# Kernel optimization log

Measured on AMD Instinct MI355X. Metric: run time of the kernel, lower is better.

Reference implementation:

```python
import jax, jax.numpy as jnp
import numpy as np

NUM_ITEMS = 100000
HIDDEN = 128
NNZ = 1600000


def setup_inputs() -> dict:
    key = jax.random.key(0)
    k1, k2, k3, k4, k5, k6 = jax.random.split(key, 6)
    item_embedding_table = jax.random.normal(k1, (NUM_ITEMS, HIDDEN), dtype=jnp.float32)
    adj_rows = jnp.sort(jax.random.randint(k2, (NNZ,), 0, NUM_ITEMS, dtype=jnp.int32))
    adj_cols = jax.random.randint(k3, (NNZ,), 0, NUM_ITEMS, dtype=jnp.int32)
    adj_vals = jax.random.uniform(k4, (NNZ,), dtype=jnp.float32)
    # nn.Linear default init (uniform in +-1/sqrt(fan_in)) approximated by scaled normal
    W_weight = jax.random.normal(k5, (HIDDEN, HIDDEN), dtype=jnp.float32) / np.sqrt(HIDDEN)
    W_bias = jax.random.normal(k6, (HIDDEN,), dtype=jnp.float32) * 0.01
    return {
        "item_embedding_table": item_embedding_table,
        "adj_rows": adj_rows,
        "adj_cols": adj_cols,
        "adj_vals": adj_vals,
        "W_weight": W_weight,
        "W_bias": W_bias,
    }


def reference(item_embedding_table, adj_rows, adj_cols, adj_vals, W_weight, W_bias):
    # support = W(x): x @ W^T + b   (nn.Linear convention: weight [out, in])
    support = jnp.einsum("nd,hd->nh", item_embedding_table, W_weight) + W_bias  # [N, H]
    # output = sparse_coo(adj) @ support, via gather + segment-sum scatter
    msgs = adj_vals[:, None] * support[adj_cols]  # [nnz, H]
    output = jax.ops.segment_sum(msgs, adj_rows, num_segments=NUM_ITEMS)  # [N, H]
    return output
```

## Files before the change

### kernel.cpp

```cpp
#include <hip/hip_runtime.h>
#include <hip/hip_fp16.h>

#define N_ITEMS 100000
#define HID 128
#define NNZ_T 1600000
#define PREPW_BLOCKS 64
#define RP_BLOCKS 391

typedef unsigned short ushort_t;
typedef unsigned int uint_t;
typedef short bf16x8 __attribute__((ext_vector_type(8)));
typedef float f32x4 __attribute__((ext_vector_type(4)));

static __device__ __forceinline__ ushort_t f32_to_bf16(float f) {
    uint_t u = __float_as_uint(f);
    uint_t r = (u + 0x7FFFu + ((u >> 16) & 1u)) >> 16;
    return (ushort_t)r;
}

__global__ void prep(const float* __restrict__ W, const int* __restrict__ rows,
                     ushort_t* __restrict__ Wb, int* __restrict__ row_ptr) {
    if (blockIdx.x < PREPW_BLOCKS) {
        int i = blockIdx.x * 256 + threadIdx.x;
        Wb[i] = f32_to_bf16(W[i]);
        return;
    }
    int r = (blockIdx.x - PREPW_BLOCKS) * 256 + threadIdx.x;
    if (r > N_ITEMS) return;
    int lo = 0, hi = NNZ_T;
    while (lo < hi) {
        int mid = (lo + hi) >> 1;
        if (rows[mid] < r) lo = mid + 1; else hi = mid;
    }
    row_ptr[r] = lo;
}

__global__ __launch_bounds__(256) void gemm_mfma(
    const float* __restrict__ X, const ushort_t* __restrict__ Wb,
    const float* __restrict__ bias, ushort_t* __restrict__ S) {
    const int lane = threadIdx.x & 63;
    const int wave = threadIdx.x >> 6;
    const int m = lane & 15;
    const int q = lane >> 4;
    const int row0 = blockIdx.x * 64 + wave * 16;

    int arow = row0 + m;
    if (arow >= N_ITEMS) arow = N_ITEMS - 1;

    f32x4 acc[8] = {};

#pragma unroll
    for (int kb = 0; kb < 4; ++kb) {
        const int k0 = kb * 32 + q * 8;
        float4 a0 = *(const float4*)&X[(size_t)arow * HID + k0];
        float4 a1 = *(const float4*)&X[(size_t)arow * HID + k0 + 4];
        bf16x8 xf;
        xf[0] = (short)f32_to_bf16(a0.x); xf[1] = (short)f32_to_bf16(a0.y);
        xf[2] = (short)f32_to_bf16(a0.z); xf[3] = (short)f32_to_bf16(a0.w);
        xf[4] = (short)f32_to_bf16(a1.x); xf[5] = (short)f32_to_bf16(a1.y);
        xf[6] = (short)f32_to_bf16(a1.z); xf[7] = (short)f32_to_bf16(a1.w);
#pragma unroll
        for (int nt = 0; nt < 8; ++nt) {
            bf16x8 wf = *(const bf16x8*)&Wb[(size_t)(nt * 16 + m) * HID + k0];
            acc[nt] = __builtin_amdgcn_mfma_f32_16x16x32_bf16(wf, xf, acc[nt], 0, 0, 0);
        }
    }

    const int srow = row0 + m;
    const bool ok = srow < N_ITEMS;
#pragma unroll
    for (int nt = 0; nt < 8; ++nt) {
        const int c0 = nt * 16 + q * 4;
        float4 bv = *(const float4*)&bias[c0];
        ushort_t h0 = __half_as_ushort(__float2half(acc[nt][0] + bv.x));
        ushort_t h1 = __half_as_ushort(__float2half(acc[nt][1] + bv.y));
        ushort_t h2 = __half_as_ushort(__float2half(acc[nt][2] + bv.z));
        ushort_t h3 = __half_as_ushort(__float2half(acc[nt][3] + bv.w));
        uint2 pk;
        pk.x = (uint_t)h0 | ((uint_t)h1 << 16);
        pk.y = (uint_t)h2 | ((uint_t)h3 << 16);
        if (ok) *(uint2*)&S[(size_t)srow * HID + c0] = pk;
    }
}

__global__ __launch_bounds__(256) void spmm_csr(
    const int* __restrict__ cols, const float* __restrict__ vals,
    const int* __restrict__ row_ptr, const ushort_t* __restrict__ S,
    float* __restrict__ out) {
    const int lane = threadIdx.x & 63;
    const int wid = blockIdx.x * 4 + ((threadIdx.x >> 6) & 3);
    const int r0 = wid * 2;
    if (r0 >= N_ITEMS) return;

    const int g = lane >> 4;
    const int l = lane & 15;
    const int sel = lane >> 5;

    const int2 p01 = *(const int2*)&row_ptr[r0];
    const int pEb = row_ptr[r0 + 2];
    int pa = p01.x; const int pEa = p01.y;
    int pb = p01.y;

    __half2 accA[4], accB[4];
#pragma unroll
    for (int j = 0; j < 4; ++j) { accA[j] = __float2half2_rn(0.f); accB[j] = __float2half2_rn(0.f); }

    while (pa < pEa || pb < pEb) {
        const int base = sel ? pb : pa;
        const int end  = sel ? pEb : pEa;
        const int idx  = base + (lane & 15);
        const int cidx = max(min(idx, end - 1), 0);
        const int c_l  = cols[cidx];
        const float v_l = (idx < end) ? vals[cidx] : 0.f;

        uint4 uA[4], uB[4];
        float vA[4], vB[4];
#pragma unroll
        for (int t = 0; t < 4; ++t) {
            const int sa = 4 * t + g;
            const int ca = __shfl(c_l, sa, 64);
            vA[t] = __shfl(v_l, sa, 64);
            uA[t] = *(const uint4*)&S[(size_t)ca * HID + 8 * l];
            const int cb = __shfl(c_l, 32 + sa, 64);
            vB[t] = __shfl(v_l, 32 + sa, 64);
            uB[t] = *(const uint4*)&S[(size_t)cb * HID + 8 * l];
        }
#pragma unroll
        for (int t = 0; t < 4; ++t) {
            const __half2 wa = __float2half2_rn(vA[t]);
            accA[0] = __hfma2(wa, *(const __half2*)&uA[t].x, accA[0]);
            accA[1] = __hfma2(wa, *(const __half2*)&uA[t].y, accA[1]);
            accA[2] = __hfma2(wa, *(const __half2*)&uA[t].z, accA[2]);
            accA[3] = __hfma2(wa, *(const __half2*)&uA[t].w, accA[3]);
            const __half2 wb = __float2half2_rn(vB[t]);
            accB[0] = __hfma2(wb, *(const __half2*)&uB[t].x, accB[0]);
            accB[1] = __hfma2(wb, *(const __half2*)&uB[t].y, accB[1]);
            accB[2] = __hfma2(wb, *(const __half2*)&uB[t].z, accB[2]);
            accB[3] = __hfma2(wb, *(const __half2*)&uB[t].w, accB[3]);
        }
        pa = min(pa + 16, pEa);
        pb = min(pb + 16, pEb);
    }

    float fA[8], fB[8];
#pragma unroll
    for (int j = 0; j < 4; ++j) {
        fA[2 * j] = __low2float(accA[j]);  fA[2 * j + 1] = __high2float(accA[j]);
        fB[2 * j] = __low2float(accB[j]);  fB[2 * j + 1] = __high2float(accB[j]);
    }
#pragma unroll
    for (int e = 0; e < 8; ++e) {
        fA[e] += __shfl_xor(fA[e], 16, 64);
        fA[e] += __shfl_xor(fA[e], 32, 64);
        fB[e] += __shfl_xor(fB[e], 16, 64);
        fB[e] += __shfl_xor(fB[e], 32, 64);
    }
    if (g == 0) {
        float* p = &out[(size_t)r0 * HID + 8 * l];
        *(float4*)p       = make_float4(fA[0], fA[1], fA[2], fA[3]);
        *(float4*)(p + 4) = make_float4(fA[4], fA[5], fA[6], fA[7]);
    } else if (g == 1 && r0 + 1 < N_ITEMS) {
        float* p = &out[(size_t)(r0 + 1) * HID + 8 * l];
        *(float4*)p       = make_float4(fB[0], fB[1], fB[2], fB[3]);
        *(float4*)(p + 4) = make_float4(fB[4], fB[5], fB[6], fB[7]);
    }
}

extern "C" void kernel_launch(void* const* d_in, const int* in_sizes, int n_in,
                              void* d_out, int out_size, void* d_ws, size_t ws_size,
                              hipStream_t stream) {
    const float* X    = (const float*)d_in[0];
    const int*   rows = (const int*)  d_in[1];
    const int*   cols = (const int*)  d_in[2];
    const float* vals = (const float*)d_in[3];
    const float* W    = (const float*)d_in[4];
    const float* bias = (const float*)d_in[5];
    float* out = (float*)d_out;

    ushort_t* Wb      = (ushort_t*)d_ws;
    ushort_t* S       = Wb + HID * HID;
    int*      row_ptr = (int*)(S + (size_t)N_ITEMS * HID);

    prep<<<PREPW_BLOCKS + RP_BLOCKS, 256, 0, stream>>>(W, rows, Wb, row_ptr);
    gemm_mfma<<<(N_ITEMS + 63) / 64, 256, 0, stream>>>(X, Wb, bias, S);
    spmm_csr<<<(N_ITEMS / 2 + 3) / 4, 256, 0, stream>>>(cols, vals, row_ptr, S, out);
}
```

Before: 203.1 us.

## Fuse prep into GEMM with LDS-staged W; persistent prefetching SpMM

Merges the W-conversion/row_ptr kernel with the GEMM so there is one fewer launch. Each GEMM block converts W to bf16 into swizzled shared memory instead of reading a global bf16 copy. The SpMM becomes a persistent grid-stride kernel that prefetches the next row pair's row_ptr and the next chunk's cols/vals while processing the current chunk, hiding index-load latency. The cost is redundant W conversion in every GEMM block, 32KB of LDS per block, and a fixed 2048-block SpMM grid that may balance load less evenly.

Measured after the change: 188.5 us. 1.08x faster.

```diff
diff --git a/kernel.cpp b/kernel.cpp
--- a/kernel.cpp
+++ b/kernel.cpp
@@ -4,8 +4,10 @@
 #define N_ITEMS 100000
 #define HID 128
 #define NNZ_T 1600000
-#define PREPW_BLOCKS 64
 #define RP_BLOCKS 391
+#define GB_BLOCKS 1563
+#define SPMM_BLOCKS 2048
+#define WSTRIDE (SPMM_BLOCKS * 4)
 
 typedef unsigned short ushort_t;
 typedef unsigned int uint_t;
@@ -18,35 +20,52 @@
     return (ushort_t)r;
 }
 
-__global__ void prep(const float* __restrict__ W, const int* __restrict__ rows,
-                     ushort_t* __restrict__ Wb, int* __restrict__ row_ptr) {
-    if (blockIdx.x < PREPW_BLOCKS) {
-        int i = blockIdx.x * 256 + threadIdx.x;
-        Wb[i] = f32_to_bf16(W[i]);
+__global__ __launch_bounds__(256) void prep_gemm(
+    const float* __restrict__ X, const float* __restrict__ W,
+    const float* __restrict__ bias, const int* __restrict__ rows,
+    ushort_t* __restrict__ S, int* __restrict__ row_ptr) {
+    if (blockIdx.x < RP_BLOCKS) {
+        int r = blockIdx.x * 256 + threadIdx.x;
+        if (r > N_ITEMS) return;
+        int lo = 0, hi = NNZ_T;
+        while (lo < hi) {
+            int mid = (lo + hi) >> 1;
+            if (rows[mid] < r) lo = mid + 1; else hi = mid;
+        }
+        row_ptr[r] = lo;
         return;
     }
-    int r = (blockIdx.x - PREPW_BLOCKS) * 256 + threadIdx.x;
-    if (r > N_ITEMS) return;
-    int lo = 0, hi = NNZ_T;
-    while (lo < hi) {
-        int mid = (lo + hi) >> 1;
-        if (rows[mid] < r) lo = mid + 1; else hi = mid;
-    }
-    row_ptr[r] = lo;
-}
-
-__global__ __launch_bounds__(256) void gemm_mfma(
-    const float* __restrict__ X, const ushort_t* __restrict__ Wb,
-    const float* __restrict__ bias, ushort_t* __restrict__ S) {
+
+    __shared__ ushort_t Wl[HID * HID];
+    {
+        const int t = threadIdx.x;
+        const float4* Wf = (const float4*)W;
+#pragma unroll
+        for (int j = 0; j < 8; ++j) {
+            const int gblk = j * 256 + t;
+            float4 w0 = Wf[gblk * 2];
+            float4 w1 = Wf[gblk * 2 + 1];
+            bf16x8 v;
+            v[0] = (short)f32_to_bf16(w0.x); v[1] = (short)f32_to_bf16(w0.y);
+            v[2] = (short)f32_to_bf16(w0.z); v[3] = (short)f32_to_bf16(w0.w);
+            v[4] = (short)f32_to_bf16(w1.x); v[5] = (short)f32_to_bf16(w1.y);
+            v[6] = (short)f32_to_bf16(w1.z); v[7] = (short)f32_to_bf16(w1.w);
+            const int ps = (gblk * 8) ^ (((gblk >> 4) & 7) << 3);
+            *(bf16x8*)&Wl[ps] = v;
+        }
+    }
+    __syncthreads();
+
     const int lane = threadIdx.x & 63;
     const int wave = threadIdx.x >> 6;
     const int m = lane & 15;
     const int q = lane >> 4;
-    const int row0 = blockIdx.x * 64 + wave * 16;
+    const int row0 = (blockIdx.x - RP_BLOCKS) * 64 + wave * 16;
 
     int arow = row0 + m;
     if (arow >= N_ITEMS) arow = N_ITEMS - 1;
 
+    const int swz = (m & 7) << 3;
     f32x4 acc[8] = {};
 
 #pragma unroll
@@ -61,7 +80,7 @@
         xf[6] = (short)f32_to_bf16(a1.z); xf[7] = (short)f32_to_bf16(a1.w);
 #pragma unroll
         for (int nt = 0; nt < 8; ++nt) {
-            bf16x8 wf = *(const bf16x8*)&Wb[(size_t)(nt * 16 + m) * HID + k0];
+            const bf16x8 wf = *(const bf16x8*)&Wl[((nt * 16 + m) * HID + k0) ^ swz];
             acc[nt] = __builtin_amdgcn_mfma_f32_16x16x32_bf16(wf, xf, acc[nt], 0, 0, 0);
         }
     }
@@ -88,81 +107,110 @@
     const int* __restrict__ row_ptr, const ushort_t* __restrict__ S,
     float* __restrict__ out) {
     const int lane = threadIdx.x & 63;
-    const int wid = blockIdx.x * 4 + ((threadIdx.x >> 6) & 3);
-    const int r0 = wid * 2;
-    if (r0 >= N_ITEMS) return;
-
     const int g = lane >> 4;
     const int l = lane & 15;
     const int sel = lane >> 5;
-
-    const int2 p01 = *(const int2*)&row_ptr[r0];
-    const int pEb = row_ptr[r0 + 2];
-    int pa = p01.x; const int pEa = p01.y;
-    int pb = p01.y;
-
-    __half2 accA[4], accB[4];
-#pragma unroll
-    for (int j = 0; j < 4; ++j) { accA[j] = __float2half2_rn(0.f); accB[j] = __float2half2_rn(0.f); }
-
-    while (pa < pEa || pb < pEb) {
-        const int base = sel ? pb : pa;
-        const int end  = sel ? pEb : pEa;
-        const int idx  = base + (lane & 15);
-        const int cidx = max(min(idx, end - 1), 0);
-        const int c_l  = cols[cidx];
-        const float v_l = (idx < end) ? vals[cidx] : 0.f;
-
-        uint4 uA[4], uB[4];
-        float vA[4], vB[4];
-#pragma unroll
-        for (int t = 0; t < 4; ++t) {
-            const int sa = 4 * t + g;
-            const int ca = __shfl(c_l, sa, 64);
-            vA[t] = __shfl(v_l, sa, 64);
-            uA[t] = *(const uint4*)&S[(size_t)ca * HID + 8 * l];
-            const int cb = __shfl(c_l, 32 + sa, 64);
-            vB[t] = __shfl(v_l, 32 + sa, 64);
-            uB[t] = *(const uint4*)&S[(size_t)cb * HID + 8 * l];
-        }
-#pragma unroll
-        for (int t = 0; t < 4; ++t) {
-            const __half2 wa = __float2half2_rn(vA[t]);
-            accA[0] = __hfma2(wa, *(const __half2*)&uA[t].x, accA[0]);
-            accA[1] = __hfma2(wa, *(const __half2*)&uA[t].y, accA[1]);
-            accA[2] = __hfma2(wa, *(const __half2*)&uA[t].z, accA[2]);
-            accA[3] = __hfma2(wa, *(const __half2*)&uA[t].w, accA[3]);
-            const __half2 wb = __float2half2_rn(vB[t]);
-            accB[0] = __hfma2(wb, *(const __half2*)&uB[t].x, accB[0]);
-            accB[1] = __hfma2(wb, *(const __half2*)&uB[t].y, accB[1]);
-            accB[2] = __hfma2(wb, *(const __half2*)&uB[t].z, accB[2]);
-            accB[3] = __hfma2(wb, *(const __half2*)&uB[t].w, accB[3]);
-        }
-        pa = min(pa + 16, pEa);
-        pb = min(pb + 16, pEb);
-    }
-
-    float fA[8], fB[8];
-#pragma unroll
-    for (int j = 0; j < 4; ++j) {
-        fA[2 * j] = __low2float(accA[j]);  fA[2 * j + 1] = __high2float(accA[j]);
-        fB[2 * j] = __low2float(accB[j]);  fB[2 * j + 1] = __high2float(accB[j]);
-    }
-#pragma unroll
-    for (int e = 0; e < 8; ++e) {
-        fA[e] += __shfl_xor(fA[e], 16, 64);
-        fA[e] += __shfl_xor(fA[e], 32, 64);
-        fB[e] += __shfl_xor(fB[e], 16, 64);
-        fB[e] += __shfl_xor(fB[e], 32, 64);
-    }
-    if (g == 0) {
-        float* p = &out[(size_t)r0 * HID + 8 * l];
-        *(float4*)p       = make_float4(fA[0], fA[1], fA[2], fA[3]);
-        *(float4*)(p + 4) = make_float4(fA[4], fA[5], fA[6], fA[7]);
-    } else if (g == 1 && r0 + 1 < N_ITEMS) {
-        float* p = &out[(size_t)(r0 + 1) * HID + 8 * l];
-        *(float4*)p       = make_float4(fB[0], fB[1], fB[2], fB[3]);
-        *(float4*)(p + 4) = make_float4(fB[4], fB[5], fB[6], fB[7]);
+    const int NP = N_ITEMS / 2;
+
+    int wid = blockIdx.x * 4 + (threadIdx.x >> 6);
+    if (wid >= NP) return;
+    int2 p01 = *(const int2*)&row_ptr[wid * 2];
+    int pE2 = row_ptr[wid * 2 + 2];
+
+    for (;;) {
+        const int nwid = wid + WSTRIDE;
+        const bool has_next = (nwid < NP);
+        int2 np01 = p01; int npE2 = pE2;
+        if (has_next) {
+            np01 = *(const int2*)&row_ptr[nwid * 2];
+            npE2 = row_ptr[nwid * 2 + 2];
+        }
+
+        int pa = p01.x; const int pEa = p01.y;
+        int pb = p01.y; const int pEb = pE2;
+
+        __half2 accA[4], accB[4];
+#pragma unroll
+        for (int j = 0; j < 4; ++j) { accA[j] = __float2half2_rn(0.f); accB[j] = __float2half2_rn(0.f); }
+
+        if (pa < pEa || pb < pEb) {
+            const int base = sel ? pb : pa;
+            const int end  = sel ? pEb : pEa;
+            const int idx  = base + l;
+            const int cidx = max(min(idx, end - 1), 0);
+            int   c_l = cols[cidx];
+            float v_l = (idx < end) ? vals[cidx] : 0.f;
+
+            for (;;) {
+                const int pa2 = min(pa + 16, pEa);
+                const int pb2 = min(pb + 16, pEb);
+                const bool more = (pa2 < pEa) || (pb2 < pEb);
+                int c_n = 0; float v_n = 0.f;
+                if (more) {
+                    const int b2 = sel ? pb2 : pa2;
+                    const int e2 = sel ? pEb : pEa;
+                    const int i2 = b2 + l;
+                    const int ci2 = max(min(i2, e2 - 1), 0);
+                    c_n = cols[ci2];
+                    v_n = (i2 < e2) ? vals[ci2] : 0.f;
+                }
+
+                uint4 uA[4], uB[4];
+                float vA[4], vB[4];
+#pragma unroll
+                for (int t = 0; t < 4; ++t) {
+                    const int sa = 4 * t + g;
+                    const int ca = __shfl(c_l, sa, 64);
+                    vA[t] = __shfl(v_l, sa, 64);
+                    uA[t] = *(const uint4*)&S[(size_t)ca * HID + 8 * l];
+                    const int cb = __shfl(c_l, 32 + sa, 64);
+                    vB[t] = __shfl(v_l, 32 + sa, 64);
+                    uB[t] = *(const uint4*)&S[(size_t)cb * HID + 8 * l];
+                }
+#pragma unroll
+                for (int t = 0; t < 4; ++t) {
+                    const __half2 wa = __float2half2_rn(vA[t]);
+                    accA[0] = __hfma2(wa, *(const __half2*)&uA[t].x, accA[0]);
+                    accA[1] = __hfma2(wa, *(const __half2*)&uA[t].y, accA[1]);
+                    accA[2] = __hfma2(wa, *(const __half2*)&uA[t].z, accA[2]);
+                    accA[3] = __hfma2(wa, *(const __half2*)&uA[t].w, accA[3]);
+                    const __half2 wb = __float2half2_rn(vB[t]);
+                    accB[0] = __hfma2(wb, *(const __half2*)&uB[t].x, accB[0]);
+                    accB[1] = __hfma2(wb, *(const __half2*)&uB[t].y, accB[1]);
+                    accB[2] = __hfma2(wb, *(const __half2*)&uB[t].z, accB[2]);
+                    accB[3] = __hfma2(wb, *(const __half2*)&uB[t].w, accB[3]);
+                }
+                if (!more) break;
+                pa = pa2; pb = pb2; c_l = c_n; v_l = v_n;
+            }
+        }
+
+        float fA[8], fB[8];
+#pragma unroll
+        for (int j = 0; j < 4; ++j) {
+            fA[2 * j] = __low2float(accA[j]);  fA[2 * j + 1] = __high2float(accA[j]);
+            fB[2 * j] = __low2float(accB[j]);  fB[2 * j + 1] = __high2float(accB[j]);
+        }
+#pragma unroll
+        for (int e = 0; e < 8; ++e) {
+            fA[e] += __shfl_xor(fA[e], 16, 64);
+            fA[e] += __shfl_xor(fA[e], 32, 64);
+            fB[e] += __shfl_xor(fB[e], 16, 64);
+            fB[e] += __shfl_xor(fB[e], 32, 64);
+        }
+        const int r0 = wid * 2;
+        if (g == 0) {
+            float* p = &out[(size_t)r0 * HID + 8 * l];
+            *(float4*)p       = make_float4(fA[0], fA[1], fA[2], fA[3]);
+            *(float4*)(p + 4) = make_float4(fA[4], fA[5], fA[6], fA[7]);
+        } else if (g == 1 && r0 + 1 < N_ITEMS) {
+            float* p = &out[(size_t)(r0 + 1) * HID + 8 * l];
+            *(float4*)p       = make_float4(fB[0], fB[1], fB[2], fB[3]);
+            *(float4*)(p + 4) = make_float4(fB[4], fB[5], fB[6], fB[7]);
+        }
+
+        if (!has_next) break;
+        wid = nwid; p01 = np01; pE2 = npE2;
     }
 }
 
@@ -177,11 +225,9 @@
     const float* bias = (const float*)d_in[5];
     float* out = (float*)d_out;
 
-    ushort_t* Wb      = (ushort_t*)d_ws;
-    ushort_t* S       = Wb + HID * HID;
+    ushort_t* S       = (ushort_t*)d_ws;
     int*      row_ptr = (int*)(S + (size_t)N_ITEMS * HID);
 
-    prep<<<PREPW_BLOCKS + RP_BLOCKS, 256, 0, stream>>>(W, rows, Wb, row_ptr);
-    gemm_mfma<<<(N_ITEMS + 63) / 64, 256, 0, stream>>>(X, Wb, bias, S);
-    spmm_csr<<<(N_ITEMS / 2 + 3) / 4, 256, 0, stream>>>(cols, vals, row_ptr, S, out);
-}
+    prep_gemm<<<RP_BLOCKS + GB_BLOCKS, 256, 0, stream>>>(X, W, bias, rows, S, row_ptr);
+    spmm_csr<<<SPMM_BLOCKS, 256, 0, stream>>>(cols, vals, row_ptr, S, out);
+}
```

## Fuse prep, GEMM and SpMM into one persistent cooperative kernel with grid sync

Applied to the files above, without the earlier changes.

Merges the three kernels into a single persistent cooperative kernel. Each block builds row_ptr with a grid-stride loop, converts W to bf16 into swizzled LDS, and runs grid-strided GEMM tiles. After a grid-wide sync it runs grid-strided SpMM rows. This removes two kernel launch boundaries and the global Wb round trip, at the cost of a grid barrier, lower occupancy from the 32KB LDS and launch bounds, and every block redundantly converting W.

New measurement: 319.7 us. +57.4%, slower.

```diff
diff --git a/kernel.cpp b/kernel.cpp
--- a/kernel.cpp
+++ b/kernel.cpp
@@ -1,11 +1,14 @@
 #include <hip/hip_runtime.h>
 #include <hip/hip_fp16.h>
+#include <hip/hip_cooperative_groups.h>
+
+namespace cg = cooperative_groups;
 
 #define N_ITEMS 100000
 #define HID 128
 #define NNZ_T 1600000
-#define PREPW_BLOCKS 64
-#define RP_BLOCKS 391
+#define GEMM_TILES 1563
+#define MAX_BLOCKS 1024
 
 typedef unsigned short ushort_t;
 typedef unsigned int uint_t;
@@ -18,151 +21,165 @@
     return (ushort_t)r;
 }
 
-__global__ void prep(const float* __restrict__ W, const int* __restrict__ rows,
-                     ushort_t* __restrict__ Wb, int* __restrict__ row_ptr) {
-    if (blockIdx.x < PREPW_BLOCKS) {
-        int i = blockIdx.x * 256 + threadIdx.x;
-        Wb[i] = f32_to_bf16(W[i]);
-        return;
-    }
-    int r = (blockIdx.x - PREPW_BLOCKS) * 256 + threadIdx.x;
-    if (r > N_ITEMS) return;
-    int lo = 0, hi = NNZ_T;
-    while (lo < hi) {
-        int mid = (lo + hi) >> 1;
-        if (rows[mid] < r) lo = mid + 1; else hi = mid;
-    }
-    row_ptr[r] = lo;
-}
-
-__global__ __launch_bounds__(256) void gemm_mfma(
-    const float* __restrict__ X, const ushort_t* __restrict__ Wb,
-    const float* __restrict__ bias, ushort_t* __restrict__ S) {
-    const int lane = threadIdx.x & 63;
-    const int wave = threadIdx.x >> 6;
+__global__ __launch_bounds__(256, 4) void gcn_fused(
+    const float* __restrict__ X, const int* __restrict__ rows,
+    const int* __restrict__ cols, const float* __restrict__ vals,
+    const float* __restrict__ W, const float* __restrict__ bias,
+    ushort_t* __restrict__ S, int* __restrict__ row_ptr,
+    float* __restrict__ out, int nblocks) {
+
+    const int tid = threadIdx.x;
+    const int lane = tid & 63;
+    const int wave = tid >> 6;
+
+    for (int r = blockIdx.x * 256 + tid; r <= N_ITEMS; r += nblocks * 256) {
+        int lo = 0, hi = NNZ_T;
+        while (lo < hi) {
+            int mid = (lo + hi) >> 1;
+            if (rows[mid] < r) lo = mid + 1; else hi = mid;
+        }
+        row_ptr[r] = lo;
+    }
+
+    __shared__ ushort_t Wl[HID * HID];
+    {
+        const float4* Wf = (const float4*)W;
+#pragma unroll
+        for (int j = 0; j < 8; ++j) {
+            const int gblk = j * 256 + tid;
+            float4 w0 = Wf[gblk * 2];
+            float4 w1 = Wf[gblk * 2 + 1];
+            bf16x8 v;
+            v[0] = (short)f32_to_bf16(w0.x); v[1] = (short)f32_to_bf16(w0.y);
+            v[2] = (short)f32_to_bf16(w0.z); v[3] = (short)f32_to_bf16(w0.w);
+            v[4] = (short)f32_to_bf16(w1.x); v[5] = (short)f32_to_bf16(w1.y);
+            v[6] = (short)f32_to_bf16(w1.z); v[7] = (short)f32_to_bf16(w1.w);
+            const int ps = (gblk * 8) ^ (((gblk >> 4) & 7) << 3);
+            *(bf16x8*)&Wl[ps] = v;
+        }
+    }
+    __syncthreads();
+
     const int m = lane & 15;
     const int q = lane >> 4;
-    const int row0 = blockIdx.x * 64 + wave * 16;
-
-    int arow = row0 + m;
-    if (arow >= N_ITEMS) arow = N_ITEMS - 1;
-
-    f32x4 acc[8] = {};
-
-#pragma unroll
-    for (int kb = 0; kb < 4; ++kb) {
-        const int k0 = kb * 32 + q * 8;
-        float4 a0 = *(const float4*)&X[(size_t)arow * HID + k0];
-        float4 a1 = *(const float4*)&X[(size_t)arow * HID + k0 + 4];
-        bf16x8 xf;
-        xf[0] = (short)f32_to_bf16(a0.x); xf[1] = (short)f32_to_bf16(a0.y);
-        xf[2] = (short)f32_to_bf16(a0.z); xf[3] = (short)f32_to_bf16(a0.w);
-        xf[4] = (short)f32_to_bf16(a1.x); xf[5] = (short)f32_to_bf16(a1.y);
-        xf[6] = (short)f32_to_bf16(a1.z); xf[7] = (short)f32_to_bf16(a1.w);
+    const int swz = (m & 7) << 3;
+    for (int tile = blockIdx.x; tile < GEMM_TILES; tile += nblocks) {
+        const int row0 = tile * 64 + wave * 16;
+        int arow = row0 + m;
+        if (arow >= N_ITEMS) arow = N_ITEMS - 1;
+
+        f32x4 acc[8] = {};
+#pragma unroll
+        for (int kb = 0; kb < 4; ++kb) {
+            const int k0 = kb * 32 + q * 8;
+            float4 a0 = *(const float4*)&X[(size_t)arow * HID + k0];
+            float4 a1 = *(const float4*)&X[(size_t)arow * HID + k0 + 4];
+            bf16x8 xf;
+            xf[0] = (short)f32_to_bf16(a0.x); xf[1] = (short)f32_to_bf16(a0.y);
+            xf[2] = (short)f32_to_bf16(a0.z); xf[3] = (short)f32_to_bf16(a0.w);
+            xf[4] = (short)f32_to_bf16(a1.x); xf[5] = (short)f32_to_bf16(a1.y);
+            xf[6] = (short)f32_to_bf16(a1.z); xf[7] = (short)f32_to_bf16(a1.w);
+#pragma unroll
+            for (int nt = 0; nt < 8; ++nt) {
+                const bf16x8 wf = *(const bf16x8*)&Wl[((nt * 16 + m) * HID + k0) ^ swz];
+                acc[nt] = __builtin_amdgcn_mfma_f32_16x16x32_bf16(wf, xf, acc[nt], 0, 0, 0);
+            }
+        }
+
+        const int srow = row0 + m;
+        const bool ok = srow < N_ITEMS;
 #pragma unroll
         for (int nt = 0; nt < 8; ++nt) {
-            bf16x8 wf = *(const bf16x8*)&Wb[(size_t)(nt * 16 + m) * HID + k0];
-            acc[nt] = __builtin_amdgcn_mfma_f32_16x16x32_bf16(wf, xf, acc[nt], 0, 0, 0);
-        }
-    }
-
-    const int srow = row0 + m;
-    const bool ok = srow < N_ITEMS;
-#pragma unroll
-    for (int nt = 0; nt < 8; ++nt) {
-        const int c0 = nt * 16 + q * 4;
-        float4 bv = *(const float4*)&bias[c0];
-        ushort_t h0 = __half_as_ushort(__float2half(acc[nt][0] + bv.x));
-        ushort_t h1 = __half_as_ushort(__float2half(acc[nt][1] + bv.y));
-        ushort_t h2 = __half_as_ushort(__float2half(acc[nt][2] + bv.z));
-        ushort_t h3 = __half_as_ushort(__float2half(acc[nt][3] + bv.w));
-        uint2 pk;
-        pk.x = (uint_t)h0 | ((uint_t)h1 << 16);
-        pk.y = (uint_t)h2 | ((uint_t)h3 << 16);
-        if (ok) *(uint2*)&S[(size_t)srow * HID + c0] = pk;
-    }
-}
-
-__global__ __launch_bounds__(256) void spmm_csr(
-    const int* __restrict__ cols, const float* __restrict__ vals,
-    const int* __restrict__ row_ptr, const ushort_t* __restrict__ S,
-    float* __restrict__ out) {
-    const int lane = threadIdx.x & 63;
-    const int wid = blockIdx.x * 4 + ((threadIdx.x >> 6) & 3);
-    const int r0 = wid * 2;
-    if (r0 >= N_ITEMS) return;
+            const int c0 = nt * 16 + q * 4;
+            float4 bv = *(const float4*)&bias[c0];
+            ushort_t h0 = __half_as_ushort(__float2half(acc[nt][0] + bv.x));
+            ushort_t h1 = __half_as_ushort(__float2half(acc[nt][1] + bv.y));
+            ushort_t h2 = __half_as_ushort(__float2half(acc[nt][2] + bv.z));
+            ushort_t h3 = __half_as_ushort(__float2half(acc[nt][3] + bv.w));
+            uint2 pk;
+            pk.x = (uint_t)h0 | ((uint_t)h1 << 16);
+            pk.y = (uint_t)h2 | ((uint_t)h3 << 16);
+            if (ok) *(uint2*)&S[(size_t)srow * HID + c0] = pk;
+        }
+    }
+
+    cg::this_grid().sync();
 
     const int g = lane >> 4;
     const int l = lane & 15;
     const int sel = lane >> 5;
-
-    const int2 p01 = *(const int2*)&row_ptr[r0];
-    const int pEb = row_ptr[r0 + 2];
-    int pa = p01.x; const int pEa = p01.y;
-    int pb = p01.y;
-
-    __half2 accA[4], accB[4];
-#pragma unroll
-    for (int j = 0; j < 4; ++j) { accA[j] = __float2half2_rn(0.f); accB[j] = __float2half2_rn(0.f); }
-
-    while (pa < pEa || pb < pEb) {
-        const int base = sel ? pb : pa;
-        const int end  = sel ? pEb : pEa;
-        const int idx  = base + (lane & 15);
-        const int cidx = max(min(idx, end - 1), 0);
-        const int c_l  = cols[cidx];
-        const float v_l = (idx < end) ? vals[cidx] : 0.f;
-
-        uint4 uA[4], uB[4];
-        float vA[4], vB[4];
-#pragma unroll
-        for (int t = 0; t < 4; ++t) {
-            const int sa = 4 * t + g;
-            const int ca = __shfl(c_l, sa, 64);
-            vA[t] = __shfl(v_l, sa, 64);
-            uA[t] = *(const uint4*)&S[(size_t)ca * HID + 8 * l];
-            const int cb = __shfl(c_l, 32 + sa, 64);
-            vB[t] = __shfl(v_l, 32 + sa, 64);
-            uB[t] = *(const uint4*)&S[(size_t)cb * HID + 8 * l];
-        }
-#pragma unroll
-        for (int t = 0; t < 4; ++t) {
-            const __half2 wa = __float2half2_rn(vA[t]);
-            accA[0] = __hfma2(wa, *(const __half2*)&uA[t].x, accA[0]);
-            accA[1] = __hfma2(wa, *(const __half2*)&uA[t].y, accA[1]);
-            accA[2] = __hfma2(wa, *(const __half2*)&uA[t].z, accA[2]);
-            accA[3] = __hfma2(wa, *(const __half2*)&uA[t].w, accA[3]);
-            const __half2 wb = __float2half2_rn(vB[t]);
-            accB[0] = __hfma2(wb, *(const __half2*)&uB[t].x, accB[0]);
-            accB[1] = __hfma2(wb, *(const __half2*)&uB[t].y, accB[1]);
-            accB[2] = __hfma2(wb, *(const __half2*)&uB[t].z, accB[2]);
-            accB[3] = __hfma2(wb, *(const __half2*)&uB[t].w, accB[3]);
-        }
-        pa = min(pa + 16, pEa);
-        pb = min(pb + 16, pEb);
-    }
-
-    float fA[8], fB[8];
-#pragma unroll
-    for (int j = 0; j < 4; ++j) {
-        fA[2 * j] = __low2float(accA[j]);  fA[2 * j + 1] = __high2float(accA[j]);
-        fB[2 * j] = __low2float(accB[j]);  fB[2 * j + 1] = __high2float(accB[j]);
-    }
-#pragma unroll
-    for (int e = 0; e < 8; ++e) {
-        fA[e] += __shfl_xor(fA[e], 16, 64);
-        fA[e] += __shfl_xor(fA[e], 32, 64);
-        fB[e] += __shfl_xor(fB[e], 16, 64);
-        fB[e] += __shfl_xor(fB[e], 32, 64);
-    }
-    if (g == 0) {
-        float* p = &out[(size_t)r0 * HID + 8 * l];
-        *(float4*)p       = make_float4(fA[0], fA[1], fA[2], fA[3]);
-        *(float4*)(p + 4) = make_float4(fA[4], fA[5], fA[6], fA[7]);
-    } else if (g == 1 && r0 + 1 < N_ITEMS) {
-        float* p = &out[(size_t)(r0 + 1) * HID + 8 * l];
-        *(float4*)p       = make_float4(fB[0], fB[1], fB[2], fB[3]);
-        *(float4*)(p + 4) = make_float4(fB[4], fB[5], fB[6], fB[7]);
+    const int nwaves = nblocks * 4;
+
+    for (int wid = blockIdx.x * 4 + wave; wid < N_ITEMS / 2; wid += nwaves) {
+        const int r0 = wid * 2;
+        const int2 p01 = *(const int2*)&row_ptr[r0];
+        const int pEb = row_ptr[r0 + 2];
+        int pa = p01.x; const int pEa = p01.y;
+        int pb = p01.y;
+
+        __half2 accA[4], accB[4];
+#pragma unroll
+        for (int j = 0; j < 4; ++j) { accA[j] = __float2half2_rn(0.f); accB[j] = __float2half2_rn(0.f); }
+
+        while (pa < pEa || pb < pEb) {
+            const int base = sel ? pb : pa;
+            const int end  = sel ? pEb : pEa;
+            const int idx  = base + (lane & 15);
+            const int cidx = max(min(idx, end - 1), 0);
+            const int c_l  = cols[cidx];
+            const float v_l = (idx < end) ? vals[cidx] : 0.f;
+
+            uint4 uA[4], uB[4];
+            float vA[4], vB[4];
+#pragma unroll
+            for (int t = 0; t < 4; ++t) {
+                const int sa = 4 * t + g;
+                const int ca = __shfl(c_l, sa, 64);
+                vA[t] = __shfl(v_l, sa, 64);
+                uA[t] = *(const uint4*)&S[(size_t)ca * HID + 8 * l];
+                const int cb = __shfl(c_l, 32 + sa, 64);
+                vB[t] = __shfl(v_l, 32 + sa, 64);
+                uB[t] = *(const uint4*)&S[(size_t)cb * HID + 8 * l];
+            }
+#pragma unroll
+            for (int t = 0; t < 4; ++t) {
+                const __half2 wa = __float2half2_rn(vA[t]);
+                accA[0] = __hfma2(wa, *(const __half2*)&uA[t].x, accA[0]);
+                accA[1] = __hfma2(wa, *(const __half2*)&uA[t].y, accA[1]);
+                accA[2] = __hfma2(wa, *(const __half2*)&uA[t].z, accA[2]);
+                accA[3] = __hfma2(wa, *(const __half2*)&uA[t].w, accA[3]);
+                const __half2 wb = __float2half2_rn(vB[t]);
+                accB[0] = __hfma2(wb, *(const __half2*)&uB[t].x, accB[0]);
+                accB[1] = __hfma2(wb, *(const __half2*)&uB[t].y, accB[1]);
+                accB[2] = __hfma2(wb, *(const __half2*)&uB[t].z, accB[2]);
+                accB[3] = __hfma2(wb, *(const __half2*)&uB[t].w, accB[3]);
+            }
+            pa = min(pa + 16, pEa);
+            pb = min(pb + 16, pEb);
+        }
+
+        float fA[8], fB[8];
+#pragma unroll
+        for (int j = 0; j < 4; ++j) {
+            fA[2 * j] = __low2float(accA[j]);  fA[2 * j + 1] = __high2float(accA[j]);
+            fB[2 * j] = __low2float(accB[j]);  fB[2 * j + 1] = __high2float(accB[j]);
+        }
+#pragma unroll
+        for (int e = 0; e < 8; ++e) {
+            fA[e] += __shfl_xor(fA[e], 16, 64);
+            fA[e] += __shfl_xor(fA[e], 32, 64);
+            fB[e] += __shfl_xor(fB[e], 16, 64);
+            fB[e] += __shfl_xor(fB[e], 32, 64);
+        }
+        if (g == 0) {
+            float* p = &out[(size_t)r0 * HID + 8 * l];
+            *(float4*)p       = make_float4(fA[0], fA[1], fA[2], fA[3]);
+            *(float4*)(p + 4) = make_float4(fA[4], fA[5], fA[6], fA[7]);
+        } else if (g == 1 && r0 + 1 < N_ITEMS) {
+            float* p = &out[(size_t)(r0 + 1) * HID + 8 * l];
+            *(float4*)p       = make_float4(fB[0], fB[1], fB[2], fB[3]);
+            *(float4*)(p + 4) = make_float4(fB[4], fB[5], fB[6], fB[7]);
+        }
     }
 }
 
@@ -177,11 +194,26 @@
     const float* bias = (const float*)d_in[5];
     float* out = (float*)d_out;
 
-    ushort_t* Wb      = (ushort_t*)d_ws;
-    ushort_t* S       = Wb + HID * HID;
+    ushort_t* S       = (ushort_t*)d_ws;
     int*      row_ptr = (int*)(S + (size_t)N_ITEMS * HID);
 
-    prep<<<PREPW_BLOCKS + RP_BLOCKS, 256, 0, stream>>>(W, rows, Wb, row_ptr);
-    gemm_mfma<<<(N_ITEMS + 63) / 64, 256, 0, stream>>>(X, Wb, bias, S);
-    spmm_csr<<<(N_ITEMS / 2 + 3) / 4, 256, 0, stream>>>(cols, vals, row_ptr, S, out);
+    static int nblocks = 0;
+    if (nblocks == 0) {
+        int per_cu = 0;
+        hipOccupancyMaxActiveBlocksPerMultiprocessor(
+            &per_cu, reinterpret_cast<const void*>(gcn_fused), 256, 0);
+        int num_cu = 256;
+        hipDeviceProp_t prop;
+        if (hipGetDeviceProperties(&prop, 0) == hipSuccess && prop.multiProcessorCount > 0)
+            num_cu = prop.multiProcessorCount;
+        nblocks = (per_cu > 0 ? per_cu : 1) * num_cu;
+        if (nblocks > MAX_BLOCKS) nblocks = MAX_BLOCKS;
+        if (nblocks < 256) nblocks = 256;
+    }
+
+    void* args[] = {(void*)&X, (void*)&rows, (void*)&cols, (void*)&vals,
+                    (void*)&W, (void*)&bias, (void*)&S, (void*)&row_ptr,
+                    (void*)&out, (void*)&nblocks};
+    hipLaunchCooperativeKernel(reinterpret_cast<void*>(gcn_fused),
+                               dim3(nblocks), dim3(256), args, 0, stream);
 }
```

## Fuse row-pointer prep and GEMM into one persistent kernel with LDS weights

Applied to the files above, without the earlier changes.

Merges the prep and GEMM launches into one kernel. Some blocks compute CSR row pointers while the rest convert W to bf16 into swizzled shared memory and loop persistently over GEMM tiles. This removes one kernel launch and the global bf16 weight buffer. Nontemporal loads and stores are also added for X, the gathered S rows and the output. The risk is that nontemporal hints on the gathered S rows lower cache reuse, and each GEMM block pays a 32KB LDS fill.

New measurement: 208.1 us. 2.5% more time.

```diff
diff --git a/kernel.cpp b/kernel.cpp
--- a/kernel.cpp
+++ b/kernel.cpp
@@ -4,13 +4,17 @@
 #define N_ITEMS 100000
 #define HID 128
 #define NNZ_T 1600000
-#define PREPW_BLOCKS 64
 #define RP_BLOCKS 391
+#define GEMM_TILES 1563
+#define GEMM_BLOCKS 781
+#define SPMM_BLOCKS 12500
 
 typedef unsigned short ushort_t;
 typedef unsigned int uint_t;
 typedef short bf16x8 __attribute__((ext_vector_type(8)));
 typedef float f32x4 __attribute__((ext_vector_type(4)));
+typedef float f32x4v __attribute__((ext_vector_type(4)));
+typedef uint_t u32x4v __attribute__((ext_vector_type(4)));
 
 static __device__ __forceinline__ ushort_t f32_to_bf16(float f) {
     uint_t u = __float_as_uint(f);
@@ -18,68 +22,90 @@
     return (ushort_t)r;
 }
 
-__global__ void prep(const float* __restrict__ W, const int* __restrict__ rows,
-                     ushort_t* __restrict__ Wb, int* __restrict__ row_ptr) {
-    if (blockIdx.x < PREPW_BLOCKS) {
-        int i = blockIdx.x * 256 + threadIdx.x;
-        Wb[i] = f32_to_bf16(W[i]);
+static __device__ __forceinline__ __half2 u2h2(uint_t w) {
+    union { uint_t u; __half2 h; } c; c.u = w; return c.h;
+}
+
+__global__ __launch_bounds__(256) void prep_gemm(
+    const float* __restrict__ X, const float* __restrict__ W,
+    const float* __restrict__ bias, const int* __restrict__ rows,
+    ushort_t* __restrict__ S, int* __restrict__ row_ptr) {
+    if (blockIdx.x < RP_BLOCKS) {
+        int r = blockIdx.x * 256 + threadIdx.x;
+        if (r > N_ITEMS) return;
+        int lo = 0, hi = NNZ_T;
+        while (lo < hi) {
+            int mid = (lo + hi) >> 1;
+            if (rows[mid] < r) lo = mid + 1; else hi = mid;
+        }
+        row_ptr[r] = lo;
         return;
     }
-    int r = (blockIdx.x - PREPW_BLOCKS) * 256 + threadIdx.x;
-    if (r > N_ITEMS) return;
-    int lo = 0, hi = NNZ_T;
-    while (lo < hi) {
-        int mid = (lo + hi) >> 1;
-        if (rows[mid] < r) lo = mid + 1; else hi = mid;
-    }
-    row_ptr[r] = lo;
-}
-
-__global__ __launch_bounds__(256) void gemm_mfma(
-    const float* __restrict__ X, const ushort_t* __restrict__ Wb,
-    const float* __restrict__ bias, ushort_t* __restrict__ S) {
+
+    __shared__ ushort_t Wl[HID * HID];
+    {
+        const int t = threadIdx.x;
+        const float4* Wf = (const float4*)W;
+#pragma unroll
+        for (int j = 0; j < 8; ++j) {
+            const int gblk = j * 256 + t;
+            float4 w0 = Wf[gblk * 2];
+            float4 w1 = Wf[gblk * 2 + 1];
+            bf16x8 v;
+            v[0] = (short)f32_to_bf16(w0.x); v[1] = (short)f32_to_bf16(w0.y);
+            v[2] = (short)f32_to_bf16(w0.z); v[3] = (short)f32_to_bf16(w0.w);
+            v[4] = (short)f32_to_bf16(w1.x); v[5] = (short)f32_to_bf16(w1.y);
+            v[6] = (short)f32_to_bf16(w1.z); v[7] = (short)f32_to_bf16(w1.w);
+            const int ps = (gblk * 8) ^ (((gblk >> 4) & 7) << 3);
+            *(bf16x8*)&Wl[ps] = v;
+        }
+    }
+    __syncthreads();
+
     const int lane = threadIdx.x & 63;
     const int wave = threadIdx.x >> 6;
     const int m = lane & 15;
     const int q = lane >> 4;
-    const int row0 = blockIdx.x * 64 + wave * 16;
-
-    int arow = row0 + m;
-    if (arow >= N_ITEMS) arow = N_ITEMS - 1;
-
-    f32x4 acc[8] = {};
-
-#pragma unroll
-    for (int kb = 0; kb < 4; ++kb) {
-        const int k0 = kb * 32 + q * 8;
-        float4 a0 = *(const float4*)&X[(size_t)arow * HID + k0];
-        float4 a1 = *(const float4*)&X[(size_t)arow * HID + k0 + 4];
-        bf16x8 xf;
-        xf[0] = (short)f32_to_bf16(a0.x); xf[1] = (short)f32_to_bf16(a0.y);
-        xf[2] = (short)f32_to_bf16(a0.z); xf[3] = (short)f32_to_bf16(a0.w);
-        xf[4] = (short)f32_to_bf16(a1.x); xf[5] = (short)f32_to_bf16(a1.y);
-        xf[6] = (short)f32_to_bf16(a1.z); xf[7] = (short)f32_to_bf16(a1.w);
+    const int swz = (m & 7) << 3;
+
+    for (int tile = blockIdx.x - RP_BLOCKS; tile < GEMM_TILES; tile += GEMM_BLOCKS) {
+        const int row0 = tile * 64 + wave * 16;
+        int arow = row0 + m;
+        if (arow >= N_ITEMS) arow = N_ITEMS - 1;
+
+        f32x4 acc[8] = {};
+#pragma unroll
+        for (int kb = 0; kb < 4; ++kb) {
+            const int k0 = kb * 32 + q * 8;
+            f32x4v a0 = __builtin_nontemporal_load((const f32x4v*)&X[(size_t)arow * HID + k0]);
+            f32x4v a1 = __builtin_nontemporal_load((const f32x4v*)&X[(size_t)arow * HID + k0 + 4]);
+            bf16x8 xf;
+            xf[0] = (short)f32_to_bf16(a0[0]); xf[1] = (short)f32_to_bf16(a0[1]);
+            xf[2] = (short)f32_to_bf16(a0[2]); xf[3] = (short)f32_to_bf16(a0[3]);
+            xf[4] = (short)f32_to_bf16(a1[0]); xf[5] = (short)f32_to_bf16(a1[1]);
+            xf[6] = (short)f32_to_bf16(a1[2]); xf[7] = (short)f32_to_bf16(a1[3]);
+#pragma unroll
+            for (int nt = 0; nt < 8; ++nt) {
+                const bf16x8 wf = *(const bf16x8*)&Wl[((nt * 16 + m) * HID + k0) ^ swz];
+                acc[nt] = __builtin_amdgcn_mfma_f32_16x16x32_bf16(wf, xf, acc[nt], 0, 0, 0);
+            }
+        }
+
+        const int srow = row0 + m;
+        const bool ok = srow < N_ITEMS;
 #pragma unroll
         for (int nt = 0; nt < 8; ++nt) {
-            bf16x8 wf = *(const bf16x8*)&Wb[(size_t)(nt * 16 + m) * HID + k0];
-            acc[nt] = __builtin_amdgcn_mfma_f32_16x16x32_bf16(wf, xf, acc[nt], 0, 0, 0);
-        }
-    }
-
-    const int srow = row0 + m;
-    const bool ok = srow < N_ITEMS;
-#pragma unroll
-    for (int nt = 0; nt < 8; ++nt) {
-        const int c0 = nt * 16 + q * 4;
-        float4 bv = *(const float4*)&bias[c0];
-        ushort_t h0 = __half_as_ushort(__float2half(acc[nt][0] + bv.x));
-        ushort_t h1 = __half_as_ushort(__float2half(acc[nt][1] + bv.y));
-        ushort_t h2 = __half_as_ushort(__float2half(acc[nt][2] + bv.z));
-        ushort_t h3 = __half_as_ushort(__float2half(acc[nt][3] + bv.w));
-        uint2 pk;
-        pk.x = (uint_t)h0 | ((uint_t)h1 << 16);
-        pk.y = (uint_t)h2 | ((uint_t)h3 << 16);
-        if (ok) *(uint2*)&S[(size_t)srow * HID + c0] = pk;
+            const int c0 = nt * 16 + q * 4;
+            float4 bv = *(const float4*)&bias[c0];
+            ushort_t h0 = __half_as_ushort(__float2half(acc[nt][0] + bv.x));
+            ushort_t h1 = __half_as_ushort(__float2half(acc[nt][1] + bv.y));
+            ushort_t h2 = __half_as_ushort(__float2half(acc[nt][2] + bv.z));
+            ushort_t h3 = __half_as_ushort(__float2half(acc[nt][3] + bv.w));
+            uint2 pk;
+            pk.x = (uint_t)h0 | ((uint_t)h1 << 16);
+            pk.y = (uint_t)h2 | ((uint_t)h3 << 16);
+            if (ok) *(uint2*)&S[(size_t)srow * HID + c0] = pk;
+        }
     }
 }
 
@@ -113,30 +139,30 @@
         const int c_l  = cols[cidx];
         const float v_l = (idx < end) ? vals[cidx] : 0.f;
 
-        uint4 uA[4], uB[4];
+        u32x4v uA[4], uB[4];
         float vA[4], vB[4];
 #pragma unroll
         for (int t = 0; t < 4; ++t) {
             const int sa = 4 * t + g;
             const int ca = __shfl(c_l, sa, 64);
             vA[t] = __shfl(v_l, sa, 64);
-            uA[t] = *(const uint4*)&S[(size_t)ca * HID + 8 * l];
+            uA[t] = __builtin_nontemporal_load((const u32x4v*)&S[(size_t)ca * HID + 8 * l]);
             const int cb = __shfl(c_l, 32 + sa, 64);
             vB[t] = __shfl(v_l, 32 + sa, 64);
-            uB[t] = *(const uint4*)&S[(size_t)cb * HID + 8 * l];
+            uB[t] = __builtin_nontemporal_load((const u32x4v*)&S[(size_t)cb * HID + 8 * l]);
         }
 #pragma unroll
         for (int t = 0; t < 4; ++t) {
             const __half2 wa = __float2half2_rn(vA[t]);
-            accA[0] = __hfma2(wa, *(const __half2*)&uA[t].x, accA[0]);
-            accA[1] = __hfma2(wa, *(const __half2*)&uA[t].y, accA[1]);
-            accA[2] = __hfma2(wa, *(const __half2*)&uA[t].z, accA[2]);
-            accA[3] = __hfma2(wa, *(const __half2*)&uA[t].w, accA[3]);
+            accA[0] = __hfma2(wa, u2h2(uA[t][0]), accA[0]);
+            accA[1] = __hfma2(wa, u2h2(uA[t][1]), accA[1]);
+            accA[2] = __hfma2(wa, u2h2(uA[t][2]), accA[2]);
+            accA[3] = __hfma2(wa, u2h2(uA[t][3]), accA[3]);
             const __half2 wb = __float2half2_rn(vB[t]);
-            accB[0] = __hfma2(wb, *(const __half2*)&uB[t].x, accB[0]);
-            accB[1] = __hfma2(wb, *(const __half2*)&uB[t].y, accB[1]);
-            accB[2] = __hfma2(wb, *(const __half2*)&uB[t].z, accB[2]);
-            accB[3] = __hfma2(wb, *(const __half2*)&uB[t].w, accB[3]);
+            accB[0] = __hfma2(wb, u2h2(uB[t][0]), accB[0]);
+            accB[1] = __hfma2(wb, u2h2(uB[t][1]), accB[1]);
+            accB[2] = __hfma2(wb, u2h2(uB[t][2]), accB[2]);
+            accB[3] = __hfma2(wb, u2h2(uB[t][3]), accB[3]);
         }
         pa = min(pa + 16, pEa);
         pb = min(pb + 16, pEb);
@@ -157,12 +183,16 @@
     }
     if (g == 0) {
         float* p = &out[(size_t)r0 * HID + 8 * l];
-        *(float4*)p       = make_float4(fA[0], fA[1], fA[2], fA[3]);
-        *(float4*)(p + 4) = make_float4(fA[4], fA[5], fA[6], fA[7]);
+        f32x4v o0; o0[0] = fA[0]; o0[1] = fA[1]; o0[2] = fA[2]; o0[3] = fA[3];
+        f32x4v o1; o1[0] = fA[4]; o1[1] = fA[5]; o1[2] = fA[6]; o1[3] = fA[7];
+        __builtin_nontemporal_store(o0, (f32x4v*)p);
+        __builtin_nontemporal_store(o1, (f32x4v*)(p + 4));
     } else if (g == 1 && r0 + 1 < N_ITEMS) {
         float* p = &out[(size_t)(r0 + 1) * HID + 8 * l];
-        *(float4*)p       = make_float4(fB[0], fB[1], fB[2], fB[3]);
-        *(float4*)(p + 4) = make_float4(fB[4], fB[5], fB[6], fB[7]);
+        f32x4v o0; o0[0] = fB[0]; o0[1] = fB[1]; o0[2] = fB[2]; o0[3] = fB[3];
+        f32x4v o1; o1[0] = fB[4]; o1[1] = fB[5]; o1[2] = fB[6]; o1[3] = fB[7];
+        __builtin_nontemporal_store(o0, (f32x4v*)p);
+        __builtin_nontemporal_store(o1, (f32x4v*)(p + 4));
     }
 }
 
@@ -177,11 +207,9 @@
     const float* bias = (const float*)d_in[5];
     float* out = (float*)d_out;
 
-    ushort_t* Wb      = (ushort_t*)d_ws;
-    ushort_t* S       = Wb + HID * HID;
+    ushort_t* S       = (ushort_t*)d_ws;
     int*      row_ptr = (int*)(S + (size_t)N_ITEMS * HID);
 
-    prep<<<PREPW_BLOCKS + RP_BLOCKS, 256, 0, stream>>>(W, rows, Wb, row_ptr);
-    gemm_mfma<<<(N_ITEMS + 63) / 64, 256, 0, stream>>>(X, Wb, bias, S);
-    spmm_csr<<<(N_ITEMS / 2 + 3) / 4, 256, 0, stream>>>(cols, vals, row_ptr, S, out);
-}
+    prep_gemm<<<RP_BLOCKS + GEMM_BLOCKS, 256, 0, stream>>>(X, W, bias, rows, S, row_ptr);
+    spmm_csr<<<SPMM_BLOCKS, 256, 0, stream>>>(cols, vals, row_ptr, S, out);
+}
```
